# Optimization experiments

Hardware: AMD Instinct MI355X
Metric: run time of the kernel (lower is better)

The kernel has to match this reference:

```python
import jax, jax.numpy as jnp
import numpy as np

NUM_HEADS = 16
NUM_HIDDENS = 1024
D_K = NUM_HIDDENS // NUM_HEADS
NEG_INF = -1.0e9


def setup_inputs() -> dict:
    key = jax.random.key(0)
    kx, kq, kk, kv, ko, kl = jax.random.split(key, 6)
    B, S, D = 2, 2048, NUM_HIDDENS
    scale = 1.0 / np.sqrt(D)
    return {
        "X": jax.random.normal(kx, (B, S, D), dtype=jnp.float32),
        "valid_lens": jax.random.randint(kl, (B,), 0, S, dtype=jnp.int64),
        "W_q": jax.random.normal(kq, (D, D), dtype=jnp.float32) * scale,
        "W_k": jax.random.normal(kk, (D, D), dtype=jnp.float32) * scale,
        "W_v": jax.random.normal(kv, (D, D), dtype=jnp.float32) * scale,
        "W_o": jax.random.normal(ko, (D, D), dtype=jnp.float32) * scale,
    }


def _split_heads(x):
    # [B, S, D] -> [B, H, S, d_k]
    B, S, _ = x.shape
    return x.reshape(B, S, NUM_HEADS, D_K).transpose(0, 2, 1, 3)


def reference(X, valid_lens, W_q, W_k, W_v, W_o):
    B, S, D = X.shape
    # nn.Linear(bias=False): y = x @ W.T  (W is [out, in])
    Q = _split_heads(jnp.einsum("bsd,ed->bse", X, W_q))  # [B,H,S,dk]
    K = _split_heads(jnp.einsum("bsd,ed->bse", X, W_k))
    V = _split_heads(jnp.einsum("bsd,ed->bse", X, W_v))

    scores = jnp.einsum("bhqd,bhkd->bhqk", Q, K) / jnp.sqrt(
        jnp.asarray(D_K, dtype=X.dtype)
    )  # [B,H,S,S]

    # key-position mask per batch: positions >= valid_len get -1e9
    mask = jnp.arange(S)[None, :] >= valid_lens[:, None]  # [B,S]
    scores = jnp.where(mask[:, None, None, :], jnp.asarray(NEG_INF, X.dtype), scores)

    attn = jax.nn.softmax(scores, axis=-1)  # dropout p=0 -> identity
    out = jnp.einsum("bhqk,bhkd->bhqd", attn, V)  # [B,H,S,dk]
    out = out.transpose(0, 2, 1, 3).reshape(B, S, D)
    return jnp.einsum("bsd,ed->bse", out, W_o)
```

## Files before the change

### kernel.cpp

```cpp
#include <hip/hip_runtime.h>
#include <stdint.h>

#define S_LEN 2048
#define BATCH 2
#define DMODEL 1024
#define NHEAD 16
#define DK 64
#define MROWS (BATCH * S_LEN)

typedef __attribute__((ext_vector_type(8))) short bf16x8;
typedef __attribute__((ext_vector_type(4))) float f32x4;
typedef __attribute__((ext_vector_type(4))) short short4v;
typedef __attribute__((ext_vector_type(2))) uint32_t u32x2;

#define VMCNT(N) asm volatile("s_waitcnt vmcnt(" #N ")" ::: "memory")

__device__ __forceinline__ short f2b(float f) {
    union { float f; uint32_t u; } c; c.f = f;
    uint32_t u = c.u;
    return (short)((u + 0x7fffu + ((u >> 16) & 1u)) >> 16);
}

__device__ __forceinline__ void gload16(const void* g, void* l) {
    __builtin_amdgcn_global_load_lds(
        (const __attribute__((address_space(1))) void*)g,
        (__attribute__((address_space(3))) void*)l, 16, 0, 0);
}

__global__ void cvt_kernel(const float* __restrict__ X, const float* __restrict__ Wq,
                           const float* __restrict__ Wk, const float* __restrict__ Wv,
                           const float* __restrict__ Wo,
                           short* __restrict__ Xb, short* __restrict__ Wqb,
                           short* __restrict__ Wkb, short* __restrict__ Wvb,
                           short* __restrict__ Wob) {
    const float* src; short* dst; int n4;
    switch (blockIdx.y) {
        case 0:  src = X;  dst = Xb;  n4 = MROWS * DMODEL / 4;  break;
        case 1:  src = Wq; dst = Wqb; n4 = DMODEL * DMODEL / 4; break;
        case 2:  src = Wk; dst = Wkb; n4 = DMODEL * DMODEL / 4; break;
        case 3:  src = Wv; dst = Wvb; n4 = DMODEL * DMODEL / 4; break;
        default: src = Wo; dst = Wob; n4 = DMODEL * DMODEL / 4; break;
    }
    for (int i = blockIdx.x * blockDim.x + threadIdx.x; i < n4;
         i += gridDim.x * blockDim.x) {
        float4 v = ((const float4*)src)[i];
        short4v o;
        o[0] = f2b(v.x); o[1] = f2b(v.y); o[2] = f2b(v.z); o[3] = f2b(v.w);
        ((short4v*)dst)[i] = o;
    }
}

template <int OUT_F32>
__global__ __launch_bounds__(256) void gemm_bt(
    const short* __restrict__ A,
    const short* __restrict__ Bt0, const short* __restrict__ Bt1,
    const short* __restrict__ Bt2,
    short* __restrict__ Cb0, short* __restrict__ Cb1, short* __restrict__ Cb2,
    float* __restrict__ Cf, int M, int N, int K) {
    __shared__ short sA[3][128 * 32];
    __shared__ short sB[3][128 * 32];

    const short* Bt = Bt0;
    short* Cb = Cb0;
    if (blockIdx.z == 1) { Bt = Bt1; Cb = Cb1; }
    else if (blockIdx.z == 2) { Bt = Bt2; Cb = Cb2; }

    const int tid = threadIdx.x;
    const int lane = tid & 63;
    const int wid = tid >> 6;
    const int wr = wid >> 1, wc = wid & 1;
    const int brow = blockIdx.y * 128;
    const int bcol = blockIdx.x * 128;
    const int lr = lane & 15;
    const int kh = (lane >> 4) << 3;
    const int swg = ((lr >> 1) & 3) << 3;
    const int khs = kh ^ swg;

    f32x4 acc[4][4] = {};

    const int idx0 = tid, idx1 = tid + 256;
    const int ar0 = idx0 >> 2, ak0 = ((idx0 & 3) << 3) ^ (((ar0 >> 1) & 3) << 3);
    const int ar1 = idx1 >> 2, ak1 = ((idx1 & 3) << 3) ^ (((ar1 >> 1) & 3) << 3);

    const short* gA0 = A + (size_t)(brow + ar0) * K + ak0;
    const short* gA1 = A + (size_t)(brow + ar1) * K + ak1;
    const short* gB0 = Bt + (size_t)(bcol + ar0) * K + ak0;
    const short* gB1 = Bt + (size_t)(bcol + ar1) * K + ak1;

#define G_STAGE(KT, PA, PB)                                   \
    do {                                                      \
        const int k0_ = (KT) << 5;                            \
        gload16(gA0 + k0_, (PA) + idx0 * 8);                  \
        gload16(gA1 + k0_, (PA) + idx1 * 8);                  \
        gload16(gB0 + k0_, (PB) + idx0 * 8);                  \
        gload16(gB1 + k0_, (PB) + idx1 * 8);                  \
    } while (0)

    const int nk = K >> 5;
    short* pA0 = &sA[0][0]; short* pA1 = &sA[1][0]; short* pA2 = &sA[2][0];
    short* pB0 = &sB[0][0]; short* pB1 = &sB[1][0]; short* pB2 = &sB[2][0];

    G_STAGE(0, pA0, pB0);
    G_STAGE(1, pA1, pB1);

    for (int kt = 0; kt < nk; ++kt) {
        if (kt == nk - 1) { VMCNT(0); } else { VMCNT(4); }
        __builtin_amdgcn_s_barrier();
        if (kt + 2 < nk) G_STAGE(kt + 2, pA2, pB2);

        bf16x8 a[4], b[4];
#pragma unroll
        for (int mt = 0; mt < 4; ++mt)
            a[mt] = *(const bf16x8*)&pA0[(wr * 64 + mt * 16 + lr) * 32 + khs];
#pragma unroll
        for (int nt = 0; nt < 4; ++nt)
            b[nt] = *(const bf16x8*)&pB0[(wc * 64 + nt * 16 + lr) * 32 + khs];
        __builtin_amdgcn_s_setprio(1);
#pragma unroll
        for (int mt = 0; mt < 4; ++mt)
#pragma unroll
            for (int nt = 0; nt < 4; ++nt)
                acc[mt][nt] = __builtin_amdgcn_mfma_f32_16x16x32_bf16(
                    a[mt], b[nt], acc[mt][nt], 0, 0, 0);
        __builtin_amdgcn_s_setprio(0);

        short* tA = pA0; pA0 = pA1; pA1 = pA2; pA2 = tA;
        short* tB = pB0; pB0 = pB1; pB1 = pB2; pB2 = tB;
    }
#undef G_STAGE

    const int rbase = (lane >> 4) << 2;
    const bool vtrans = (!OUT_F32) && (blockIdx.z == 2);
#pragma unroll
    for (int mt = 0; mt < 4; ++mt) {
#pragma unroll
        for (int nt = 0; nt < 4; ++nt) {
            if (vtrans) {
                int row0 = brow + wr * 64 + mt * 16 + rbase;
                int col = bcol + wc * 64 + nt * 16 + lr;
                int bb = row0 >> 11, key = row0 & 2047;
                int hh = col >> 6, d = col & 63;
                short4v pk;
#pragma unroll
                for (int j = 0; j < 4; ++j) pk[j] = f2b(acc[mt][nt][j]);
                *(short4v*)&Cb[((size_t)((bb * 16 + hh) * 64 + d)) * S_LEN + key] = pk;
            } else {
#pragma unroll
                for (int j = 0; j < 4; ++j) {
                    int row = brow + wr * 64 + mt * 16 + rbase + j;
                    int col = bcol + wc * 64 + nt * 16 + lr;
                    if (OUT_F32)
                        Cf[(size_t)row * N + col] = acc[mt][nt][j];
                    else
                        Cb[(size_t)row * N + col] = f2b(acc[mt][nt][j]);
                }
            }
        }
    }
}

__global__ __launch_bounds__(256) void attn_kernel(
    const short* __restrict__ Q, const short* __restrict__ K,
    const short* __restrict__ Vt, short* __restrict__ O,
    const int* __restrict__ vlens) {
    __shared__ short sK[3][64 * 64];
    __shared__ short sV[3][64 * 64];
    __shared__ short sP[4][2][16 * 64];

    const int tid = threadIdx.x;
    const int lane = tid & 63;
    const int w = tid >> 6;
    const int id = blockIdx.x;
    const int xcd = id & 7;
    const int r = id >> 3;
    const int b = (r >> 5) & 1;
    const int h = (xcd << 1) | (r & 1);
    const int qb = (r >> 1) & 15;
    const int lr = lane & 15;
    const int kh = (lane >> 4) << 3;
    const int rbase = (lane >> 4) << 2;
    const int swq = (lr & 7) << 3;

    int vl = vlens[b];
    if (vl < 0) vl = 0;
    if (vl > S_LEN) vl = S_LEN;
    const bool allm = (vl == 0);
    if (allm) vl = S_LEN;
    const int nT = (vl + 63) >> 6;
    const int nFull = ((vl & 63) == 0) ? nT : nT - 1;

    const size_t rowbase = (size_t)(b * S_LEN) * DMODEL + h * DK;
    const short* vt = Vt + ((size_t)((b * 16 + h) * 64)) * S_LEN;

    const short* qrowA = Q + rowbase + (size_t)(qb * 128 + w * 32 + lr) * DMODEL;
    const short* qrowB = qrowA + 16 * DMODEL;
    bf16x8 qf0a = *(const bf16x8*)(qrowA + kh);
    bf16x8 qf1a = *(const bf16x8*)(qrowA + 32 + kh);
    bf16x8 qf0b = *(const bf16x8*)(qrowB + kh);
    bf16x8 qf1b = *(const bf16x8*)(qrowB + 32 + kh);
    if (allm) {
#pragma unroll
        for (int i = 0; i < 8; ++i) { qf0a[i] = 0; qf1a[i] = 0; qf0b[i] = 0; qf1b[i] = 0; }
    }

    f32x4 oacA[4] = {}, oacB[4] = {};
    float mA = -1e30f, mcA = -1e30f, lA = 0.f;
    float mB = -1e30f, mcB = -1e30f, lB = 0.f;
    const float CEXP = 0.18033688011112042f;
    const float THRADD = 44.361419556f;

    const int lofs0 = lr * 64 + (kh ^ swq);
    const int lofs1 = lr * 64 + ((32 + kh) ^ swq);

    const int kr = tid >> 3;
    const int kc = (((tid & 7) ^ (kr & 7)) << 3);
    const short* kBase = K + rowbase + (size_t)kr * DMODEL + kc;
    const short* vBase = vt + (size_t)kr * S_LEN + kc;

#define A_STAGE(T, PK, PV)                                                      \
    do {                                                                        \
        const short* kg_ = kBase + (size_t)((T) * 64) * DMODEL;                 \
        gload16(kg_, (PK) + tid * 8);                                           \
        gload16(kg_ + (size_t)32 * DMODEL, (PK) + (tid + 256) * 8);             \
        const short* vg_ = vBase + (T) * 64;                                    \
        gload16(vg_, (PV) + tid * 8);                                           \
        gload16(vg_ + (size_t)32 * S_LEN, (PV) + (tid + 256) * 8);              \
    } while (0)

#define SOFTMAX_FRAG(SACC, MRUN, MC, LRUN, OAC, SPW)                            \
    do {                                                                        \
        float t0 = fmaxf(fmaxf(SACC[0][0], SACC[0][1]), SACC[0][2]);            \
        float t1 = fmaxf(fmaxf(SACC[0][3], SACC[1][0]), SACC[1][1]);            \
        float t2 = fmaxf(fmaxf(SACC[1][2], SACC[1][3]), SACC[2][0]);            \
        float t3 = fmaxf(fmaxf(SACC[2][1], SACC[2][2]), SACC[2][3]);            \
        float t4 = fmaxf(fmaxf(SACC[3][0], SACC[3][1]), SACC[3][2]);            \
        float pmax = fmaxf(fmaxf(fmaxf(t0, t1), t2),                            \
                           fmaxf(fmaxf(t3, t4), SACC[3][3]));                   \
        if (__any(pmax > MRUN + THRADD)) {                                      \
            float mx = pmax;                                                    \
            mx = fmaxf(mx, __shfl_xor(mx, 16));                                 \
            mx = fmaxf(mx, __shfl_xor(mx, 32));                                 \
            float scl = __builtin_exp2f((MRUN - mx) * CEXP);                    \
            MRUN = mx;                                                          \
            MC = mx * CEXP;                                                     \
            LRUN *= scl;                                                        \
            _Pragma("unroll")                                                   \
            for (int dt = 0; dt < 4; ++dt)                                      \
                _Pragma("unroll")                                               \
                for (int j = 0; j < 4; ++j) OAC[dt][j] *= scl;                  \
        }                                                                       \
        float p[16];                                                            \
        _Pragma("unroll")                                                       \
        for (int nt = 0; nt < 4; ++nt)                                          \
            _Pragma("unroll")                                                   \
            for (int j = 0; j < 4; ++j)                                         \
                p[nt * 4 + j] = __builtin_exp2f(                                \
                    __builtin_fmaf(SACC[nt][j], CEXP, -MC));                    \
        float ls = ((p[0] + p[1]) + (p[2] + p[3])) +                            \
                   ((p[4] + p[5]) + (p[6] + p[7]));                             \
        ls += ((p[8] + p[9]) + (p[10] + p[11])) +                               \
              ((p[12] + p[13]) + (p[14] + p[15]));                              \
        LRUN += ls;                                                             \
        _Pragma("unroll")                                                       \
        for (int nt = 0; nt < 4; ++nt) {                                        \
            u32x2 r_;                                                           \
            asm("v_cvt_pk_bf16_f32 %0, %1, %2"                                  \
                : "=v"(r_[0]) : "v"(p[nt * 4 + 0]), "v"(p[nt * 4 + 1]));        \
            asm("v_cvt_pk_bf16_f32 %0, %1, %2"                                  \
                : "=v"(r_[1]) : "v"(p[nt * 4 + 2]), "v"(p[nt * 4 + 3]));        \
            *(u32x2*)&SPW[lr * 64 + ((nt * 16 + rbase) ^ swq)] = r_;            \
        }                                                                       \
    } while (0)

#define TILE_BODY(MASKED_C, PK, PV)                                             \
    do {                                                                        \
        constexpr bool MASKED = MASKED_C;                                       \
        const short* kL0 = (PK) + lofs0;                                        \
        const short* kL1 = (PK) + lofs1;                                        \
        f32x4 saccA[4] = {}, saccB[4] = {};                                     \
        __builtin_amdgcn_s_setprio(1);                                          \
        _Pragma("unroll")                                                       \
        for (int nt = 0; nt < 4; ++nt) {                                        \
            bf16x8 kb0 = *(const bf16x8*)&kL0[nt * 1024];                       \
            bf16x8 kb1 = *(const bf16x8*)&kL1[nt * 1024];                       \
            saccA[nt] = __builtin_amdgcn_mfma_f32_16x16x32_bf16(                \
                kb0, qf0a, saccA[nt], 0, 0, 0);                                 \
            saccB[nt] = __builtin_amdgcn_mfma_f32_16x16x32_bf16(                \
                kb0, qf0b, saccB[nt], 0, 0, 0);                                 \
            saccA[nt] = __builtin_amdgcn_mfma_f32_16x16x32_bf16(                \
                kb1, qf1a, saccA[nt], 0, 0, 0);                                 \
            saccB[nt] = __builtin_amdgcn_mfma_f32_16x16x32_bf16(                \
                kb1, qf1b, saccB[nt], 0, 0, 0);                                 \
        }                                                                       \
        __builtin_amdgcn_s_setprio(0);                                          \
        if (MASKED) {                                                           \
            _Pragma("unroll")                                                   \
            for (int nt = 0; nt < 4; ++nt)                                      \
                _Pragma("unroll")                                               \
                for (int j = 0; j < 4; ++j) {                                   \
                    int keyi = t * 64 + nt * 16 + rbase + j;                    \
                    if (keyi >= vl) { saccA[nt][j] = -3.0e38f;                  \
                                      saccB[nt][j] = -3.0e38f; }                \
                }                                                               \
        }                                                                       \
        SOFTMAX_FRAG(saccA, mA, mcA, lA, oacA, (&sP[w][0][0]));                 \
        SOFTMAX_FRAG(saccB, mB, mcB, lB, oacB, (&sP[w][1][0]));                 \
        const short* vL0 = (PV) + lofs0;                                        \
        const short* vL1 = (PV) + lofs1;                                        \
        __builtin_amdgcn_s_setprio(1);                                          \
        {                                                                       \
            bf16x8 pfA = *(const bf16x8*)&sP[w][0][lofs0];                      \
            bf16x8 pfB = *(const bf16x8*)&sP[w][1][lofs0];                      \
            _Pragma("unroll")                                                   \
            for (int dt = 0; dt < 4; ++dt) {                                    \
                bf16x8 vf = *(const bf16x8*)&vL0[dt * 1024];                    \
                oacA[dt] = __builtin_amdgcn_mfma_f32_16x16x32_bf16(             \
                    vf, pfA, oacA[dt], 0, 0, 0);                                \
                oacB[dt] = __builtin_amdgcn_mfma_f32_16x16x32_bf16(             \
                    vf, pfB, oacB[dt], 0, 0, 0);                                \
            }                                                                   \
            pfA = *(const bf16x8*)&sP[w][0][lofs1];                             \
            pfB = *(const bf16x8*)&sP[w][1][lofs1];                             \
            _Pragma("unroll")                                                   \
            for (int dt = 0; dt < 4; ++dt) {                                    \
                bf16x8 vf = *(const bf16x8*)&vL1[dt * 1024];                    \
                oacA[dt] = __builtin_amdgcn_mfma_f32_16x16x32_bf16(             \
                    vf, pfA, oacA[dt], 0, 0, 0);                                \
                oacB[dt] = __builtin_amdgcn_mfma_f32_16x16x32_bf16(             \
                    vf, pfB, oacB[dt], 0, 0, 0);                                \
            }                                                                   \
        }                                                                       \
        __builtin_amdgcn_s_setprio(0);                                          \
    } while (0)

    short* pK0 = &sK[0][0]; short* pK1 = &sK[1][0]; short* pK2 = &sK[2][0];
    short* pV0 = &sV[0][0]; short* pV1 = &sV[1][0]; short* pV2 = &sV[2][0];

    A_STAGE(0, pK0, pV0);
    if (nT > 1) A_STAGE(1, pK1, pV1);

    for (int t = 0; t < nT; ++t) {
        if (t == nT - 1) { VMCNT(0); } else { VMCNT(4); }
        __builtin_amdgcn_s_barrier();
        if (t + 2 < nT) A_STAGE(t + 2, pK2, pV2);

        if (t < nFull) TILE_BODY(false, pK0, pV0);
        else TILE_BODY(true, pK0, pV0);

        short* tK = pK0; pK0 = pK1; pK1 = pK2; pK2 = tK;
        short* tV = pV0; pV0 = pV1; pV1 = pV2; pV2 = tV;
    }
#undef TILE_BODY
#undef SOFTMAX_FRAG
#undef A_STAGE

    float ltA = lA + __shfl_xor(lA, 16);
    ltA += __shfl_xor(ltA, 32);
    float rlA = 1.f / ltA;
    float ltB = lB + __shfl_xor(lB, 16);
    ltB += __shfl_xor(ltB, 32);
    float rlB = 1.f / ltB;

    short* orowA = O + rowbase + (size_t)(qb * 128 + w * 32 + lr) * DMODEL;
    short* orowB = orowA + 16 * DMODEL;
#pragma unroll
    for (int dt = 0; dt < 4; ++dt) {
        short4v pkA, pkB;
#pragma unroll
        for (int j = 0; j < 4; ++j) {
            pkA[j] = f2b(oacA[dt][j] * rlA);
            pkB[j] = f2b(oacB[dt][j] * rlB);
        }
        *(short4v*)&orowA[dt * 16 + rbase] = pkA;
        *(short4v*)&orowB[dt * 16 + rbase] = pkB;
    }
}

extern "C" void kernel_launch(void* const* d_in, const int* in_sizes, int n_in,
                              void* d_out, int out_size, void* d_ws, size_t ws_size,
                              hipStream_t stream) {
    const float* X = (const float*)d_in[0];
    const int* vlens = (const int*)d_in[1];
    const float* Wq = (const float*)d_in[2];
    const float* Wk = (const float*)d_in[3];
    const float* Wv = (const float*)d_in[4];
    const float* Wo = (const float*)d_in[5];
    float* out = (float*)d_out;

    short* Xb = (short*)d_ws;
    short* Wqb = Xb + (size_t)MROWS * DMODEL;
    short* Wkb = Wqb + (size_t)DMODEL * DMODEL;
    short* Wvb = Wkb + (size_t)DMODEL * DMODEL;
    short* Wob = Wvb + (size_t)DMODEL * DMODEL;
    short* Qb = Wob + (size_t)DMODEL * DMODEL;
    short* Kb = Qb + (size_t)MROWS * DMODEL;
    short* Vtb = Kb + (size_t)MROWS * DMODEL;
    short* Ob = Vtb + (size_t)MROWS * DMODEL;

    cvt_kernel<<<dim3(512, 5), 256, 0, stream>>>(X, Wq, Wk, Wv, Wo, Xb, Wqb, Wkb,
                                                 Wvb, Wob);
    gemm_bt<0><<<dim3(8, 32, 3), 256, 0, stream>>>(Xb, Wqb, Wkb, Wvb, Qb, Kb, Vtb,
                                                   nullptr, MROWS, DMODEL, DMODEL);
    attn_kernel<<<dim3(512), 256, 0, stream>>>(Qb, Kb, Vtb, Ob, vlens);
    gemm_bt<1><<<dim3(8, 32, 1), 256, 0, stream>>>(Ob, Wob, Wob, Wob, nullptr,
                                                   nullptr, nullptr, out, MROWS,
                                                   DMODEL, DMODEL);
}
```

Before: 104.5 us.

## Switch attention to 32x32x16 MFMA with register-only P via permlane32 swap

Rewrites the attention inner loop to use 32x32x16 bf16 MFMAs instead of 16x16x32. Each lane now owns one query row, which simplifies the softmax reductions. The probability tile is repacked into MFMA operand layout in registers with v_permlane32_swap, removing the per-warp LDS round-trip for P. Launch bounds now request 3 blocks per CU, which may constrain registers given the larger 16-float accumulators.

```diff
diff --git a/kernel.cpp b/kernel.cpp
--- a/kernel.cpp
+++ b/kernel.cpp
@@ -10,8 +10,8 @@
 
 typedef __attribute__((ext_vector_type(8))) short bf16x8;
 typedef __attribute__((ext_vector_type(4))) float f32x4;
+typedef __attribute__((ext_vector_type(16))) float f32x16;
 typedef __attribute__((ext_vector_type(4))) short short4v;
-typedef __attribute__((ext_vector_type(2))) uint32_t u32x2;
 
 #define VMCNT(N) asm volatile("s_waitcnt vmcnt(" #N ")" ::: "memory")
 
@@ -159,13 +159,12 @@
     }
 }
 
-__global__ __launch_bounds__(256) void attn_kernel(
+__global__ __launch_bounds__(256, 3) void attn_kernel(
     const short* __restrict__ Q, const short* __restrict__ K,
     const short* __restrict__ Vt, short* __restrict__ O,
     const int* __restrict__ vlens) {
     __shared__ short sK[3][64 * 64];
     __shared__ short sV[3][64 * 64];
-    __shared__ short sP[4][2][16 * 64];
 
     const int tid = threadIdx.x;
     const int lane = tid & 63;
@@ -176,10 +175,9 @@
     const int b = (r >> 5) & 1;
     const int h = (xcd << 1) | (r & 1);
     const int qb = (r >> 1) & 15;
-    const int lr = lane & 15;
-    const int kh = (lane >> 4) << 3;
-    const int rbase = (lane >> 4) << 2;
-    const int swq = (lr & 7) << 3;
+    const int rl_ = lane & 31;
+    const int g = lane >> 5;
+    const int sw = (lane & 7) << 3;
 
     int vl = vlens[b];
     if (vl < 0) vl = 0;
@@ -192,25 +190,28 @@
     const size_t rowbase = (size_t)(b * S_LEN) * DMODEL + h * DK;
     const short* vt = Vt + ((size_t)((b * 16 + h) * 64)) * S_LEN;
 
-    const short* qrowA = Q + rowbase + (size_t)(qb * 128 + w * 32 + lr) * DMODEL;
-    const short* qrowB = qrowA + 16 * DMODEL;
-    bf16x8 qf0a = *(const bf16x8*)(qrowA + kh);
-    bf16x8 qf1a = *(const bf16x8*)(qrowA + 32 + kh);
-    bf16x8 qf0b = *(const bf16x8*)(qrowB + kh);
-    bf16x8 qf1b = *(const bf16x8*)(qrowB + 32 + kh);
+    const int q = qb * 128 + w * 32 + rl_;
+    const short* qA = Q + rowbase + (size_t)q * DMODEL;
+    bf16x8 qf[4];
+#pragma unroll
+    for (int f = 0; f < 4; ++f)
+        qf[f] = *(const bf16x8*)(qA + f * 16 + g * 8);
     if (allm) {
 #pragma unroll
-        for (int i = 0; i < 8; ++i) { qf0a[i] = 0; qf1a[i] = 0; qf0b[i] = 0; qf1b[i] = 0; }
-    }
-
-    f32x4 oacA[4] = {}, oacB[4] = {};
-    float mA = -1e30f, mcA = -1e30f, lA = 0.f;
-    float mB = -1e30f, mcB = -1e30f, lB = 0.f;
+        for (int f = 0; f < 4; ++f)
+#pragma unroll
+            for (int i = 0; i < 8; ++i) qf[f][i] = 0;
+    }
+
+    f32x16 oac0 = {}, oac1 = {};
+    float m_run = -1e30f, mc = -1e30f, l_run = 0.f;
     const float CEXP = 0.18033688011112042f;
     const float THRADD = 44.361419556f;
 
-    const int lofs0 = lr * 64 + (kh ^ swq);
-    const int lofs1 = lr * 64 + ((32 + kh) ^ swq);
+    int lofs[4];
+#pragma unroll
+    for (int f = 0; f < 4; ++f)
+        lofs[f] = rl_ * 64 + (((f * 16) + g * 8) ^ sw);
 
     const int kr = tid >> 3;
     const int kc = (((tid & 7) ^ (kr & 7)) << 3);
@@ -227,108 +228,93 @@
         gload16(vg_ + (size_t)32 * S_LEN, (PV) + (tid + 256) * 8);              \
     } while (0)
 
-#define SOFTMAX_FRAG(SACC, MRUN, MC, LRUN, OAC, SPW)                            \
-    do {                                                                        \
-        float t0 = fmaxf(fmaxf(SACC[0][0], SACC[0][1]), SACC[0][2]);            \
-        float t1 = fmaxf(fmaxf(SACC[0][3], SACC[1][0]), SACC[1][1]);            \
-        float t2 = fmaxf(fmaxf(SACC[1][2], SACC[1][3]), SACC[2][0]);            \
-        float t3 = fmaxf(fmaxf(SACC[2][1], SACC[2][2]), SACC[2][3]);            \
-        float t4 = fmaxf(fmaxf(SACC[3][0], SACC[3][1]), SACC[3][2]);            \
-        float pmax = fmaxf(fmaxf(fmaxf(t0, t1), t2),                            \
-                           fmaxf(fmaxf(t3, t4), SACC[3][3]));                   \
-        if (__any(pmax > MRUN + THRADD)) {                                      \
-            float mx = pmax;                                                    \
-            mx = fmaxf(mx, __shfl_xor(mx, 16));                                 \
-            mx = fmaxf(mx, __shfl_xor(mx, 32));                                 \
-            float scl = __builtin_exp2f((MRUN - mx) * CEXP);                    \
-            MRUN = mx;                                                          \
-            MC = mx * CEXP;                                                     \
-            LRUN *= scl;                                                        \
-            _Pragma("unroll")                                                   \
-            for (int dt = 0; dt < 4; ++dt)                                      \
-                _Pragma("unroll")                                               \
-                for (int j = 0; j < 4; ++j) OAC[dt][j] *= scl;                  \
-        }                                                                       \
-        float p[16];                                                            \
-        _Pragma("unroll")                                                       \
-        for (int nt = 0; nt < 4; ++nt)                                          \
-            _Pragma("unroll")                                                   \
-            for (int j = 0; j < 4; ++j)                                         \
-                p[nt * 4 + j] = __builtin_exp2f(                                \
-                    __builtin_fmaf(SACC[nt][j], CEXP, -MC));                    \
-        float ls = ((p[0] + p[1]) + (p[2] + p[3])) +                            \
-                   ((p[4] + p[5]) + (p[6] + p[7]));                             \
-        ls += ((p[8] + p[9]) + (p[10] + p[11])) +                               \
-              ((p[12] + p[13]) + (p[14] + p[15]));                              \
-        LRUN += ls;                                                             \
-        _Pragma("unroll")                                                       \
-        for (int nt = 0; nt < 4; ++nt) {                                        \
-            u32x2 r_;                                                           \
-            asm("v_cvt_pk_bf16_f32 %0, %1, %2"                                  \
-                : "=v"(r_[0]) : "v"(p[nt * 4 + 0]), "v"(p[nt * 4 + 1]));        \
-            asm("v_cvt_pk_bf16_f32 %0, %1, %2"                                  \
-                : "=v"(r_[1]) : "v"(p[nt * 4 + 2]), "v"(p[nt * 4 + 3]));        \
-            *(u32x2*)&SPW[lr * 64 + ((nt * 16 + rbase) ^ swq)] = r_;            \
-        }                                                                       \
-    } while (0)
+#define MK_FRAG(A0, A1, A2, A3)                                                 \
+    ({ union { uint32_t u[4]; bf16x8 v; } _f;                                   \
+       _f.u[0] = (A0); _f.u[1] = (A1); _f.u[2] = (A2); _f.u[3] = (A3); _f.v; })
 
 #define TILE_BODY(MASKED_C, PK, PV)                                             \
     do {                                                                        \
         constexpr bool MASKED = MASKED_C;                                       \
-        const short* kL0 = (PK) + lofs0;                                        \
-        const short* kL1 = (PK) + lofs1;                                        \
-        f32x4 saccA[4] = {}, saccB[4] = {};                                     \
+        f32x16 s0 = {}, s1 = {};                                                \
         __builtin_amdgcn_s_setprio(1);                                          \
         _Pragma("unroll")                                                       \
-        for (int nt = 0; nt < 4; ++nt) {                                        \
-            bf16x8 kb0 = *(const bf16x8*)&kL0[nt * 1024];                       \
-            bf16x8 kb1 = *(const bf16x8*)&kL1[nt * 1024];                       \
-            saccA[nt] = __builtin_amdgcn_mfma_f32_16x16x32_bf16(                \
-                kb0, qf0a, saccA[nt], 0, 0, 0);                                 \
-            saccB[nt] = __builtin_amdgcn_mfma_f32_16x16x32_bf16(                \
-                kb0, qf0b, saccB[nt], 0, 0, 0);                                 \
-            saccA[nt] = __builtin_amdgcn_mfma_f32_16x16x32_bf16(                \
-                kb1, qf1a, saccA[nt], 0, 0, 0);                                 \
-            saccB[nt] = __builtin_amdgcn_mfma_f32_16x16x32_bf16(                \
-                kb1, qf1b, saccB[nt], 0, 0, 0);                                 \
+        for (int f = 0; f < 4; ++f) {                                           \
+            bf16x8 ka = *(const bf16x8*)&(PK)[lofs[f]];                         \
+            bf16x8 kb2 = *(const bf16x8*)&(PK)[lofs[f] + 2048];                 \
+            s0 = __builtin_amdgcn_mfma_f32_32x32x16_bf16(ka, qf[f], s0, 0, 0, 0); \
+            s1 = __builtin_amdgcn_mfma_f32_32x32x16_bf16(kb2, qf[f], s1, 0, 0, 0); \
         }                                                                       \
         __builtin_amdgcn_s_setprio(0);                                          \
         if (MASKED) {                                                           \
             _Pragma("unroll")                                                   \
-            for (int nt = 0; nt < 4; ++nt)                                      \
-                _Pragma("unroll")                                               \
-                for (int j = 0; j < 4; ++j) {                                   \
-                    int keyi = t * 64 + nt * 16 + rbase + j;                    \
-                    if (keyi >= vl) { saccA[nt][j] = -3.0e38f;                  \
-                                      saccB[nt][j] = -3.0e38f; }                \
-                }                                                               \
-        }                                                                       \
-        SOFTMAX_FRAG(saccA, mA, mcA, lA, oacA, (&sP[w][0][0]));                 \
-        SOFTMAX_FRAG(saccB, mB, mcB, lB, oacB, (&sP[w][1][0]));                 \
-        const short* vL0 = (PV) + lofs0;                                        \
-        const short* vL1 = (PV) + lofs1;                                        \
+            for (int rg = 0; rg < 16; ++rg) {                                   \
+                int key0 = t * 64 + (rg & 3) + 8 * (rg >> 2) + 4 * g;           \
+                if (key0 >= vl) s0[rg] = -3.0e38f;                              \
+                if (key0 + 32 >= vl) s1[rg] = -3.0e38f;                         \
+            }                                                                   \
+        }                                                                       \
+        float x0 = fmaxf(fmaxf(s0[0], s0[1]), fmaxf(s0[2], s0[3]));             \
+        float x1 = fmaxf(fmaxf(s0[4], s0[5]), fmaxf(s0[6], s0[7]));             \
+        float x2 = fmaxf(fmaxf(s0[8], s0[9]), fmaxf(s0[10], s0[11]));           \
+        float x3 = fmaxf(fmaxf(s0[12], s0[13]), fmaxf(s0[14], s0[15]));         \
+        float x4 = fmaxf(fmaxf(s1[0], s1[1]), fmaxf(s1[2], s1[3]));             \
+        float x5 = fmaxf(fmaxf(s1[4], s1[5]), fmaxf(s1[6], s1[7]));             \
+        float x6 = fmaxf(fmaxf(s1[8], s1[9]), fmaxf(s1[10], s1[11]));           \
+        float x7 = fmaxf(fmaxf(s1[12], s1[13]), fmaxf(s1[14], s1[15]));         \
+        float px = fmaxf(fmaxf(fmaxf(x0, x1), fmaxf(x2, x3)),                   \
+                         fmaxf(fmaxf(x4, x5), fmaxf(x6, x7)));                  \
+        if (__any(px > m_run + THRADD)) {                                       \
+            float mx = fmaxf(px, __shfl_xor(px, 32));                           \
+            mx = fmaxf(mx, m_run);                                              \
+            float scl = __builtin_exp2f((m_run - mx) * CEXP);                   \
+            m_run = mx; mc = mx * CEXP;                                         \
+            l_run *= scl;                                                       \
+            _Pragma("unroll")                                                   \
+            for (int i = 0; i < 16; ++i) { oac0[i] *= scl; oac1[i] *= scl; }    \
+        }                                                                       \
+        uint32_t P0[8], P1[8];                                                  \
+        float ls = 0.f;                                                         \
+        _Pragma("unroll")                                                       \
+        for (int i = 0; i < 8; ++i) {                                           \
+            float a0 = __builtin_exp2f(__builtin_fmaf(s0[2 * i], CEXP, -mc));   \
+            float a1 = __builtin_exp2f(__builtin_fmaf(s0[2 * i + 1], CEXP, -mc)); \
+            float b0 = __builtin_exp2f(__builtin_fmaf(s1[2 * i], CEXP, -mc));   \
+            float b1 = __builtin_exp2f(__builtin_fmaf(s1[2 * i + 1], CEXP, -mc)); \
+            ls += (a0 + a1) + (b0 + b1);                                        \
+            asm("v_cvt_pk_bf16_f32 %0, %1, %2" : "=v"(P0[i]) : "v"(a0), "v"(a1)); \
+            asm("v_cvt_pk_bf16_f32 %0, %1, %2" : "=v"(P1[i]) : "v"(b0), "v"(b1)); \
+        }                                                                       \
+        l_run += ls;                                                            \
+        asm volatile("v_permlane32_swap_b32 %0, %1" : "+v"(P0[0]), "+v"(P0[2])); \
+        asm volatile("v_permlane32_swap_b32 %0, %1" : "+v"(P0[1]), "+v"(P0[3])); \
+        asm volatile("v_permlane32_swap_b32 %0, %1" : "+v"(P0[4]), "+v"(P0[6])); \
+        asm volatile("v_permlane32_swap_b32 %0, %1" : "+v"(P0[5]), "+v"(P0[7])); \
+        asm volatile("v_permlane32_swap_b32 %0, %1" : "+v"(P1[0]), "+v"(P1[2])); \
+        asm volatile("v_permlane32_swap_b32 %0, %1" : "+v"(P1[1]), "+v"(P1[3])); \
+        asm volatile("v_permlane32_swap_b32 %0, %1" : "+v"(P1[4]), "+v"(P1[6])); \
+        asm volatile("v_permlane32_swap_b32 %0, %1" : "+v"(P1[5]), "+v"(P1[7])); \
+        bf16x8 F0 = MK_FRAG(P0[0], P0[1], P0[2], P0[3]);                        \
+        bf16x8 F1 = MK_FRAG(P0[4], P0[5], P0[6], P0[7]);                        \
+        bf16x8 F2 = MK_FRAG(P1[0], P1[1], P1[2], P1[3]);                        \
+        bf16x8 F3 = MK_FRAG(P1[4], P1[5], P1[6], P1[7]);                        \
         __builtin_amdgcn_s_setprio(1);                                          \
         {                                                                       \
-            bf16x8 pfA = *(const bf16x8*)&sP[w][0][lofs0];                      \
-            bf16x8 pfB = *(const bf16x8*)&sP[w][1][lofs0];                      \
-            _Pragma("unroll")                                                   \
-            for (int dt = 0; dt < 4; ++dt) {                                    \
-                bf16x8 vf = *(const bf16x8*)&vL0[dt * 1024];                    \
-                oacA[dt] = __builtin_amdgcn_mfma_f32_16x16x32_bf16(             \
-                    vf, pfA, oacA[dt], 0, 0, 0);                                \
-                oacB[dt] = __builtin_amdgcn_mfma_f32_16x16x32_bf16(             \
-                    vf, pfB, oacB[dt], 0, 0, 0);                                \
-            }                                                                   \
-            pfA = *(const bf16x8*)&sP[w][0][lofs1];                             \
-            pfB = *(const bf16x8*)&sP[w][1][lofs1];                             \
-            _Pragma("unroll")                                                   \
-            for (int dt = 0; dt < 4; ++dt) {                                    \
-                bf16x8 vf = *(const bf16x8*)&vL1[dt * 1024];                    \
-                oacA[dt] = __builtin_amdgcn_mfma_f32_16x16x32_bf16(             \
-                    vf, pfA, oacA[dt], 0, 0, 0);                                \
-                oacB[dt] = __builtin_amdgcn_mfma_f32_16x16x32_bf16(             \
-                    vf, pfB, oacB[dt], 0, 0, 0);                                \
-            }                                                                   \
+            bf16x8 v0 = *(const bf16x8*)&(PV)[lofs[0]];                         \
+            bf16x8 v1 = *(const bf16x8*)&(PV)[lofs[0] + 2048];                  \
+            oac0 = __builtin_amdgcn_mfma_f32_32x32x16_bf16(v0, F0, oac0, 0, 0, 0); \
+            oac1 = __builtin_amdgcn_mfma_f32_32x32x16_bf16(v1, F0, oac1, 0, 0, 0); \
+            v0 = *(const bf16x8*)&(PV)[lofs[1]];                                \
+            v1 = *(const bf16x8*)&(PV)[lofs[1] + 2048];                         \
+            oac0 = __builtin_amdgcn_mfma_f32_32x32x16_bf16(v0, F1, oac0, 0, 0, 0); \
+            oac1 = __builtin_amdgcn_mfma_f32_32x32x16_bf16(v1, F1, oac1, 0, 0, 0); \
+            v0 = *(const bf16x8*)&(PV)[lofs[2]];                                \
+            v1 = *(const bf16x8*)&(PV)[lofs[2] + 2048];                         \
+            oac0 = __builtin_amdgcn_mfma_f32_32x32x16_bf16(v0, F2, oac0, 0, 0, 0); \
+            oac1 = __builtin_amdgcn_mfma_f32_32x32x16_bf16(v1, F2, oac1, 0, 0, 0); \
+            v0 = *(const bf16x8*)&(PV)[lofs[3]];                                \
+            v1 = *(const bf16x8*)&(PV)[lofs[3] + 2048];                         \
+            oac0 = __builtin_amdgcn_mfma_f32_32x32x16_bf16(v0, F3, oac0, 0, 0, 0); \
+            oac1 = __builtin_amdgcn_mfma_f32_32x32x16_bf16(v1, F3, oac1, 0, 0, 0); \
         }                                                                       \
         __builtin_amdgcn_s_setprio(0);                                          \
     } while (0)
@@ -351,28 +337,24 @@
         short* tV = pV0; pV0 = pV1; pV1 = pV2; pV2 = tV;
     }
 #undef TILE_BODY
-#undef SOFTMAX_FRAG
 #undef A_STAGE
-
-    float ltA = lA + __shfl_xor(lA, 16);
-    ltA += __shfl_xor(ltA, 32);
-    float rlA = 1.f / ltA;
-    float ltB = lB + __shfl_xor(lB, 16);
-    ltB += __shfl_xor(ltB, 32);
-    float rlB = 1.f / ltB;
-
-    short* orowA = O + rowbase + (size_t)(qb * 128 + w * 32 + lr) * DMODEL;
-    short* orowB = orowA + 16 * DMODEL;
-#pragma unroll
-    for (int dt = 0; dt < 4; ++dt) {
-        short4v pkA, pkB;
+#undef MK_FRAG
+
+    float lt = l_run + __shfl_xor(l_run, 32);
+    float rl2 = 1.f / lt;
+
+    short* orow = O + rowbase + (size_t)q * DMODEL;
+#pragma unroll
+    for (int r2 = 0; r2 < 4; ++r2) {
+        short4v pk0, pk1;
 #pragma unroll
         for (int j = 0; j < 4; ++j) {
-            pkA[j] = f2b(oacA[dt][j] * rlA);
-            pkB[j] = f2b(oacB[dt][j] * rlB);
+            pk0[j] = f2b(oac0[r2 * 4 + j] * rl2);
+            pk1[j] = f2b(oac1[r2 * 4 + j] * rl2);
         }
-        *(short4v*)&orowA[dt * 16 + rbase] = pkA;
-        *(short4v*)&orowB[dt * 16 + rbase] = pkB;
+        int d0 = r2 * 8 + 4 * g;
+        *(short4v*)&orow[d0] = pk0;
+        *(short4v*)&orow[32 + d0] = pk1;
     }
 }
 
```

Result: slower. 107.3 us (+2.7%).
